# Performance work log

Hardware: AMD Instinct MI355X
Metric: run time of the kernel (lower is better)

The kernel has to match this reference:

```python
import jax, jax.numpy as jnp
import numpy as np

B, D_in, D_hid, D_out, D_future = 1024, 1024, 1024, 512, 32


def _lin_init(key, out_d, in_d, k_scale):
    k = 1.0 / np.sqrt(k_scale)
    k1, k2 = jax.random.split(key)
    W = jax.random.uniform(k1, (out_d, in_d), minval=-k, maxval=k, dtype=jnp.float32)
    b = jax.random.uniform(k2, (out_d,), minval=-k, maxval=k, dtype=jnp.float32)
    return W, b


def _lstm_cell(x, h, c, W_ih, W_hh, b_ih, b_hh):
    # PyTorch LSTMCell gate order: i, f, g, o
    gates = x @ W_ih.T + b_ih + h @ W_hh.T + b_hh
    i, f, g, o = jnp.split(gates, 4, axis=1)
    c2 = jax.nn.sigmoid(f) * c + jax.nn.sigmoid(i) * jnp.tanh(g)
    h2 = jax.nn.sigmoid(o) * jnp.tanh(c2)
    return h2, c2


def setup_inputs() -> dict:
    key = jax.random.key(0)
    ks = jax.random.split(key, 16)
    x = jax.random.normal(ks[0], (B, D_in), dtype=jnp.float32)
    hx = jax.random.normal(ks[1], (B, D_hid), dtype=jnp.float32)
    cx = jax.random.normal(ks[2], (B, D_hid), dtype=jnp.float32)
    # Decoder LSTMCell(D_out -> D_hid); torch init scale 1/sqrt(hidden)
    W_ih_dec, b_ih_dec = _lin_init(ks[3], 4 * D_hid, D_out, D_hid)
    W_hh_dec, b_hh_dec = _lin_init(ks[4], 4 * D_hid, D_hid, D_hid)
    W_r0, b_r0 = _lin_init(ks[5], D_hid, D_hid, D_hid)
    W_rp, b_rp = _lin_init(ks[6], D_out, D_hid, D_hid)
    W_rr, b_rr = _lin_init(ks[7], D_out, D_out, D_out)
    W_s0, b_s0 = _lin_init(ks[8], D_in, D_hid, D_hid)
    # StaRNNCell LSTMCell(2*D_in -> D_hid)
    W_ih_sta, b_ih_sta = _lin_init(ks[9], 4 * D_hid, 2 * D_in, D_hid)
    W_hh_sta, b_hh_sta = _lin_init(ks[10], 4 * D_hid, D_hid, D_hid)
    W_sn, b_sn = _lin_init(ks[11], D_out, D_hid, D_hid)
    return dict(x=x, hx=hx, cx=cx,
                W_ih_dec=W_ih_dec, W_hh_dec=W_hh_dec, b_ih_dec=b_ih_dec, b_hh_dec=b_hh_dec,
                W_r0=W_r0, b_r0=b_r0, W_rp=W_rp, b_rp=b_rp, W_rr=W_rr, b_rr=b_rr,
                W_s0=W_s0, b_s0=b_s0,
                W_ih_sta=W_ih_sta, W_hh_sta=W_hh_sta, b_ih_sta=b_ih_sta, b_hh_sta=b_hh_sta,
                W_sn=W_sn, b_sn=b_sn)


def reference(x, hx, cx,
              W_ih_dec, W_hh_dec, b_ih_dec, b_hh_dec,
              W_r0, b_r0, W_rp, b_rp, W_rr, b_rr,
              W_s0, b_s0,
              W_ih_sta, W_hh_sta, b_ih_sta, b_hh_sta,
              W_sn, b_sn):
    ohx, ocx = hx, cx
    r0 = jnp.zeros((x.shape[0], D_out), dtype=x.dtype)
    hd0 = hx @ W_r0.T + b_r0  # LinLayerR0

    def step(carry, _):
        r, hd, cd = carry
        hd, cd = _lstm_cell(r, hd, cd, W_ih_dec, W_hh_dec, b_ih_dec, b_hh_dec)
        p = hd @ W_rp.T + b_rp    # LinLayerRp
        r = p @ W_rr.T + b_rr     # LinLayerRr
        return (r, hd, cd), (hd, p)

    _, (fts_bar, Act_bar) = jax.lax.scan(step, (r0, hd0, cx), None, length=D_future)
    # fts_bar: [D_future, B, D_hid]; AvgPool1d over D_future == mean over axis 0
    hbar = fts_bar.mean(axis=0)
    xbar = jax.nn.relu(hbar @ W_s0.T + b_s0)  # LinLayerS0 + relu
    xcat = jnp.concatenate([x, xbar], axis=1)
    hx2, cx2 = _lstm_cell(xcat, ohx, ocx, W_ih_sta, W_hh_sta, b_ih_sta, b_hh_sta)
    Act = hx2 @ W_sn.T + b_sn  # LinLayerSn
    return (Act, Act_bar, (hx2, cx2))
```

## Files before the change

### kernel.cpp

```cpp
#include <hip/hip_runtime.h>
#include <hip/hip_bf16.h>
#include <stdint.h>


typedef unsigned short ushort_t;
typedef __attribute__((ext_vector_type(8))) short short8;
typedef __attribute__((ext_vector_type(4))) float floatx4;

__device__ __forceinline__ unsigned short f2bf(float f) {
    unsigned int u = __float_as_uint(f);
    u += 0x7FFF + ((u >> 16) & 1);
    return (unsigned short)(u >> 16);
}
__device__ __forceinline__ float bf2f(unsigned short u) {
    return __uint_as_float(((unsigned int)u) << 16);
}
__device__ __forceinline__ float sigm(float x) { return 1.f / (1.f + __expf(-x)); }

__device__ __forceinline__ void glds16(const ushort_t* g, const ushort_t* l) {
    __builtin_amdgcn_global_load_lds(
        (const __attribute__((address_space(1))) uint32_t*)g,
        (__attribute__((address_space(3))) uint32_t*)l, 16, 0, 0);
}

__device__ __forceinline__ unsigned ld_rlx(const unsigned* p) {
    return __hip_atomic_load(p, __ATOMIC_RELAXED, __HIP_MEMORY_SCOPE_AGENT);
}

template <bool WF, bool WB, bool RELU, bool NT>
__global__ __launch_bounds__(256)
void gemm_bt(const ushort_t* __restrict__ A, int lda,
             const ushort_t* __restrict__ Bw, int ldb,
             int Kloop, int kzOff,
             const float* __restrict__ bias,
             float* __restrict__ Cf, int ldcf, size_t czStride,
             ushort_t* __restrict__ Cb, int ldcb) {
    __shared__ __align__(16) ushort_t As[128 * 32];
    __shared__ __align__(16) ushort_t Bs[128 * 32];
    const int t = threadIdx.x;
    const int l = t & 63;
    const int w = t >> 6;
    int bx = blockIdx.x, by = blockIdx.y;
    if ((gridDim.y & 7) == 0) {
        const int flat = bx + gridDim.x * by;
        const int xcd = flat & 7;
        const int j = flat >> 3;
        const int jm = j / gridDim.x;
        by = xcd * (gridDim.y >> 3) + jm;
        bx = j - jm * gridDim.x;
    }
    const int m0 = by << 7;
    const int n0 = bx << 7;
    const int kz = blockIdx.z;
    A  += (size_t)kz * kzOff;
    Bw += (size_t)kz * kzOff;
    if (WF) Cf += (size_t)kz * czStride;
    const int wm = (w >> 1) << 6;
    const int wn = (w & 1) << 6;
    const int lr = l & 15;
    const int lg = l >> 4;

    floatx4 acc[4][4] = {};

    const int srow = (w << 4) + (l >> 2);
    const int cc = ((l & 3) - ((l >> 3) & 3)) & 3;
    const int scol = cc << 3;
    const ushort_t* Ag0 = A + (size_t)(m0 + srow) * lda + scol;
    const ushort_t* Ag1 = A + (size_t)(m0 + 64 + srow) * lda + scol;
    const ushort_t* Bg0 = Bw + (size_t)(n0 + srow) * ldb + scol;
    const ushort_t* Bg1 = Bw + (size_t)(n0 + 64 + srow) * ldb + scol;
    const ushort_t* lA0 = &As[t * 8];
    const ushort_t* lA1 = &As[2048 + t * 8];
    const ushort_t* lB0 = &Bs[t * 8];
    const ushort_t* lB1 = &Bs[2048 + t * 8];

    int aoff[4], boff[4];
#pragma unroll
    for (int i = 0; i < 4; i++) {
        const int Ra = wm + i * 16 + lr;
        aoff[i] = ((Ra << 2) + ((lg + ((Ra >> 1) & 3)) & 3)) << 3;
        const int Rb = wn + i * 16 + lr;
        boff[i] = ((Rb << 2) + ((lg + ((Rb >> 1) & 3)) & 3)) << 3;
    }

    for (int kk = 0; kk < Kloop; kk += 32) {
        glds16(Ag0 + kk, lA0);
        glds16(Ag1 + kk, lA1);
        glds16(Bg0 + kk, lB0);
        glds16(Bg1 + kk, lB1);
        __syncthreads();
        short8 af[4], bfr[4];
#pragma unroll
        for (int i = 0; i < 4; i++) af[i] = *(const short8*)&As[aoff[i]];
#pragma unroll
        for (int j = 0; j < 4; j++) bfr[j] = *(const short8*)&Bs[boff[j]];
#pragma unroll
        for (int i = 0; i < 4; i++)
#pragma unroll
            for (int j = 0; j < 4; j++)
                acc[i][j] = __builtin_amdgcn_mfma_f32_16x16x32_bf16(af[i], bfr[j], acc[i][j], 0, 0, 0);
        __syncthreads();
    }

#pragma unroll
    for (int i = 0; i < 4; i++) {
#pragma unroll
        for (int j = 0; j < 4; j++) {
            const int col = n0 + wn + j * 16 + lr;
            const float bv = bias ? bias[col] : 0.f;
#pragma unroll
            for (int r = 0; r < 4; r++) {
                const int row = m0 + wm + i * 16 + lg * 4 + r;
                float v = acc[i][j][r] + bv;
                if (RELU) v = fmaxf(v, 0.f);
                if (WF) {
                    if (NT) __builtin_nontemporal_store(v, &Cf[(size_t)row * ldcf + col]);
                    else Cf[(size_t)row * ldcf + col] = v;
                }
                if (WB) Cb[(size_t)row * ldcb + col] = f2bf(v);
            }
        }
    }
}

template <bool HF, bool NT>
__global__ __launch_bounds__(256, 2)
void gates_fused(const ushort_t* __restrict__ A, int lda,
                 const ushort_t* __restrict__ WI, int K,
                 const float* __restrict__ biasI,
                 const float* __restrict__ cin, float* __restrict__ cout,
                 ushort_t* __restrict__ hbf, int ldh,
                 float* __restrict__ hf) {
    __shared__ __align__(16) float Cs[64 * 132];
    ushort_t* AsBase = (ushort_t*)Cs;
    const int t = threadIdx.x;
    const int l = t & 63;
    const int w = t >> 6;
    const int flat = blockIdx.x + (blockIdx.y << 5);
    const int xcd = flat & 7;
    const int jsw = flat >> 3;
    const int bn = (xcd << 2) + (jsw >> 4);
    const int bm = jsw & 15;
    const int m0 = bm << 6;
    const int n0 = bn << 7;
    const int u0 = bn << 5;
    const int lr = l & 15;
    const int lg = l >> 4;

    floatx4 acc[4][2] = {};

    const int srow = t >> 2;
    const int cc = ((t & 3) - ((t >> 3) & 3)) & 3;
    const int scol = cc << 3;
    const ushort_t* Ag = A + (size_t)(m0 + srow) * lda + scol;

    int aoff[4];
#pragma unroll
    for (int i = 0; i < 4; i++) {
        const int Ra = i * 16 + lr;
        aoff[i] = ((Ra << 2) + ((lg + ((Ra >> 1) & 3)) & 3)) << 3;
    }
    const ushort_t* BgW[2];
#pragma unroll
    for (int jf = 0; jf < 2; jf++)
        BgW[jf] = WI + (size_t)(n0 + (w << 5) + jf * 16 + lr) * K + (lg << 3);

    auto issueA = [&](int b, int sp) {
#pragma unroll
        for (int s = 0; s < 4; s++)
            glds16(Ag + sp * 128 + s * 32, AsBase + b * 8192 + s * 2048 + t * 8);
    };
    auto loadB = [&](short8 (&br)[4][2], int sp) {
#pragma unroll
        for (int s = 0; s < 4; s++)
#pragma unroll
            for (int jf = 0; jf < 2; jf++)
                br[s][jf] = *(const short8*)(BgW[jf] + sp * 128 + s * 32);
    };
    auto compute = [&](int b, short8 (&br)[4][2]) {
#pragma unroll
        for (int s = 0; s < 4; s++) {
            short8 af[4];
#pragma unroll
            for (int i = 0; i < 4; i++)
                af[i] = *(const short8*)(AsBase + b * 8192 + s * 2048 + aoff[i]);
#pragma unroll
            for (int i = 0; i < 4; i++)
#pragma unroll
                for (int jf = 0; jf < 2; jf++)
                    acc[i][jf] = __builtin_amdgcn_mfma_f32_16x16x32_bf16(af[i], br[s][jf], acc[i][jf], 0, 0, 0);
        }
    };

    short8 b0[4][2], b1[4][2];
    const int NS = K >> 7;
    issueA(0, 0);
    loadB(b0, 0);
    for (int sp = 0; sp < NS; sp += 2) {
        __syncthreads();
        if (sp + 1 < NS) { issueA(1, sp + 1); loadB(b1, sp + 1); }
        compute(0, b0);
        __syncthreads();
        if (sp + 2 < NS) { issueA(0, sp + 2); loadB(b0, sp + 2); }
        compute(1, b1);
    }
    __syncthreads();

#pragma unroll
    for (int i = 0; i < 4; i++)
#pragma unroll
        for (int jf = 0; jf < 2; jf++) {
            const int colb = (w << 5) + jf * 16 + lr;
#pragma unroll
            for (int r = 0; r < 4; r++)
                Cs[(i * 16 + lg * 4 + r) * 132 + colb] = acc[i][jf][r];
        }
    __syncthreads();

#pragma unroll
    for (int p = 0; p < 8; p++) {
        const int row = p * 8 + (t >> 5);
        const int uu = t & 31;
        const float4 g4 = *(const float4*)&Cs[row * 132 + uu * 4];
        const int grow = m0 + row;
        const int gu = u0 + uu;
        const float4 b4 = *(const float4*)&biasI[gu * 4];
        const float iv = sigm(g4.x + b4.x);
        const float fv = sigm(g4.y + b4.y);
        const float gv = tanhf(g4.z + b4.z);
        const float ov = sigm(g4.w + b4.w);
        const size_t cidx = (size_t)grow * 1024 + gu;
        const float c = fv * cin[cidx] + iv * gv;
        const float h = ov * tanhf(c);
        if (NT) __builtin_nontemporal_store(c, &cout[cidx]);
        else cout[cidx] = c;
        hbf[(size_t)grow * ldh + gu] = f2bf(h);
        if (HF) {
            if (NT) __builtin_nontemporal_store(h, &hf[cidx]);
            else hf[cidx] = h;
        }
    }
}

__global__ __launch_bounds__(512, 1)
void gates_rows(ushort_t* __restrict__ HD,
                const ushort_t* __restrict__ Wh,
                const ushort_t* __restrict__ Wg,
                const float* __restrict__ biasD,
                const float* __restrict__ biasG,
                const float* __restrict__ cx,
                ushort_t* __restrict__ hbarb,
                unsigned* __restrict__ flags) {
    const size_t SLOT = 1048576;
    __shared__ __align__(16) float Cs[64 * 260];
    ushort_t* AsBase = (ushort_t*)Cs;
    const int t = threadIdx.x;
    const int l = t & 63;
    const int w = t >> 6;
    const int bid = blockIdx.x;
    const int g = bid >> 4;
    const int q = bid & 15;
    const int m0 = g << 6;
    const int n0 = q << 8;
    const int u0 = q << 6;
    const int lr = l & 15;
    const int lg = l >> 4;

    const int u8 = t & 255;
    const int pr = t >> 8;
    const int srow = u8 >> 2;
    const int cc = ((u8 & 3) - ((u8 >> 3) & 3)) & 3;
    const ushort_t* Ag = HD + (size_t)(m0 + srow) * 1024 + (cc << 3);

    int aoff[4];
#pragma unroll
    for (int i = 0; i < 4; i++) {
        const int Ra = i * 16 + lr;
        aoff[i] = ((Ra << 2) + ((lg + ((Ra >> 1) & 3)) & 3)) << 3;
    }

    const int uu = t & 63;
    const int gu = u0 + uu;
    const int rb = t >> 6;
    const float4 b4d = *(const float4*)&biasD[gu * 4];
    const float4 b4g = *(const float4*)&biasG[gu * 4];
    float cst[8], hsum[8];
#pragma unroll
    for (int p = 0; p < 8; p++) {
        cst[p] = cx[(size_t)(m0 + p * 8 + rb) * 1024 + gu];
        hsum[p] = 0.f;
    }

    for (int s = 0; s < 32; ++s) {
        if (s) {
            if (t < 16)
                while (ld_rlx(&flags[((g << 4) | t) << 4]) < (unsigned)s)
                    __builtin_amdgcn_s_sleep(2);
            __syncthreads();
        }

        const ushort_t* W = s ? Wg : Wh;
        const ushort_t* BgW[2];
#pragma unroll
        for (int jf = 0; jf < 2; jf++)
            BgW[jf] = W + (size_t)(n0 + (w << 5) + jf * 16 + lr) * 1024 + (lg << 3);

        floatx4 acc[4][2] = {};

        auto issueA = [&](int b, int sp) {
#pragma unroll
            for (int j = 0; j < 2; j++) {
                const int ss = pr * 2 + j;
                glds16(Ag + sp * 128 + ss * 32,
                       AsBase + b * 8192 + ss * 2048 + u8 * 8);
            }
        };
        auto loadB = [&](short8 (&br)[4][2], int sp) {
#pragma unroll
            for (int ss = 0; ss < 4; ss++)
#pragma unroll
                for (int jf = 0; jf < 2; jf++)
                    br[ss][jf] = *(const short8*)(BgW[jf] + sp * 128 + ss * 32);
        };
        auto compute = [&](int b, short8 (&br)[4][2]) {
#pragma unroll
            for (int ss = 0; ss < 4; ss++) {
                short8 af[4];
#pragma unroll
                for (int i = 0; i < 4; i++)
                    af[i] = *(const short8*)(AsBase + b * 8192 + ss * 2048 + aoff[i]);
#pragma unroll
                for (int i = 0; i < 4; i++)
#pragma unroll
                    for (int jf = 0; jf < 2; jf++)
                        acc[i][jf] = __builtin_amdgcn_mfma_f32_16x16x32_bf16(af[i], br[ss][jf], acc[i][jf], 0, 0, 0);
            }
        };

        short8 b0[4][2], b1[4][2];
        issueA(0, 0);
        loadB(b0, 0);
        for (int sp = 0; sp < 8; sp += 2) {
            __syncthreads();
            if (sp + 1 < 8) { issueA(1, sp + 1); loadB(b1, sp + 1); }
            compute(0, b0);
            __syncthreads();
            if (sp + 2 < 8) { issueA(0, sp + 2); loadB(b0, sp + 2); }
            compute(1, b1);
        }
        __syncthreads();

#pragma unroll
        for (int i = 0; i < 4; i++)
#pragma unroll
            for (int jf = 0; jf < 2; jf++) {
                const int colb = (w << 5) + jf * 16 + lr;
#pragma unroll
                for (int r = 0; r < 4; r++)
                    Cs[(i * 16 + lg * 4 + r) * 260 + colb] = acc[i][jf][r];
            }
        __syncthreads();

        ushort_t* Hout = HD + (size_t)(s + 1) * SLOT;
        const float4 b4 = s ? b4g : b4d;
#pragma unroll
        for (int p = 0; p < 8; p++) {
            const int row = p * 8 + rb;
            const float4 g4 = *(const float4*)&Cs[row * 260 + uu * 4];
            const float iv = sigm(g4.x + b4.x);
            const float fv = sigm(g4.y + b4.y);
            const float gv = tanhf(g4.z + b4.z);
            const float ov = sigm(g4.w + b4.w);
            cst[p] = fv * cst[p] + iv * gv;
            const float h = ov * tanhf(cst[p]);
            Hout[(size_t)(m0 + row) * 1024 + gu] = f2bf(h);
            hsum[p] += h;
        }

        if (s < 31) {
            __syncthreads();
            if (t == 0)
                __hip_atomic_store(&flags[((g << 4) | q) << 4], (unsigned)(s + 1),
                                   __ATOMIC_RELEASE, __HIP_MEMORY_SCOPE_AGENT);
        }
        Ag += SLOT;
    }

#pragma unroll
    for (int p = 0; p < 8; p++)
        hbarb[(size_t)(m0 + p * 8 + rb) * 1024 + gu] = f2bf(hsum[p] * (1.f / 32.f));
}

__global__ void zero_bar(unsigned* __restrict__ b, int n) {
    int i = blockIdx.x * 256 + threadIdx.x;
    if (i < n) b[i] = 0u;
}

__global__ void pack2_bf(ushort_t* __restrict__ dst, const float* __restrict__ s1, int K1,
                         const float* __restrict__ s2, int K2) {
    const int n = blockIdx.y;
    const int k = blockIdx.x * 256 + threadIdx.x;
    const int Kt = K1 + K2;
    float v = (k < K1) ? s1[(size_t)n * K1 + k] : s2[(size_t)n * K2 + (k - K1)];
    dst[(size_t)n * Kt + k] = f2bf(v);
}

__global__ void tpose_bf(ushort_t* __restrict__ dst, const float* __restrict__ src,
                         int R, int C) {
    const int c = blockIdx.y;
    const int r = blockIdx.x * 256 + threadIdx.x;
    dst[(size_t)c * R + r] = f2bf(src[(size_t)r * C + c]);
}

__global__ void ileave_whh_k(ushort_t* __restrict__ dst, const float* __restrict__ Whh) {
    const int rI = blockIdx.y;
    const int k = blockIdx.x * 256 + threadIdx.x;
    const int r = ((rI & 3) << 10) + (rI >> 2);
    dst[(size_t)rI * 1024 + k] = f2bf(Whh[(size_t)r * 1024 + k]);
}

__global__ void ileave_add_k(ushort_t* __restrict__ dst, const float* __restrict__ Wgf,
                             const float* __restrict__ Whh) {
    const int rI = blockIdx.y;
    const int k = blockIdx.x * 256 + threadIdx.x;
    const int r = ((rI & 3) << 10) + (rI >> 2);
    dst[(size_t)rI * 1024 + k] = f2bf(Wgf[(size_t)r * 1024 + k] + Whh[(size_t)r * 1024 + k]);
}

__global__ void ileave_sta_k(ushort_t* __restrict__ dst, const float* __restrict__ Wih,
                             const float* __restrict__ Whh) {
    const int rI = blockIdx.y;
    const int k = blockIdx.x * 256 + threadIdx.x;
    const int r = ((rI & 3) << 10) + (rI >> 2);
    float v = (k < 2048) ? Wih[(size_t)r * 2048 + k] : Whh[(size_t)r * 1024 + (k - 2048)];
    dst[(size_t)rI * 3072 + k] = f2bf(v);
}

__global__ void bias_il_k(float* __restrict__ dst, const float* __restrict__ b_ih,
                          const float* __restrict__ b_hh) {
    const int rI = blockIdx.x * 256 + threadIdx.x;
    const int r = ((rI & 3) << 10) + (rI >> 2);
    dst[rI] = b_ih[r] + b_hh[r];
}

__global__ void br2_k(float* __restrict__ br2, const float* __restrict__ Wrr,
                      const float* __restrict__ b_rp, const float* __restrict__ b_rr) {
    const int o = blockIdx.x * 256 + threadIdx.x;
    float s = b_rr[o];
    for (int m = 0; m < 512; m++) s += Wrr[o * 512 + m] * b_rp[m];
    br2[o] = s;
}

__global__ void biasg_k(float* __restrict__ dst, const float* __restrict__ Wih,
                        const float* __restrict__ b_ih, const float* __restrict__ b_hh,
                        const float* __restrict__ br2) {
    const int rI = blockIdx.x * 256 + threadIdx.x;
    const int r = ((rI & 3) << 10) + (rI >> 2);
    float s = b_ih[r] + b_hh[r];
    for (int o = 0; o < 512; o++) s += Wih[(size_t)r * 512 + o] * br2[o];
    dst[rI] = s;
}

__global__ void init_sta(const float* __restrict__ x, const float* __restrict__ hx,
                         ushort_t* __restrict__ A2) {
    int idx = blockIdx.x * 256 + threadIdx.x;
    int b = idx >> 10, j = idx & 1023;
    A2[(size_t)b * 3072 + j] = f2bf(x[idx]);
    A2[(size_t)b * 3072 + 2048 + j] = f2bf(hx[idx]);
}

extern "C" void kernel_launch(void* const* d_in, const int* in_sizes, int n_in,
                              void* d_out, int out_size, void* d_ws, size_t ws_size,
                              hipStream_t stream) {
    const float* x        = (const float*)d_in[0];
    const float* hx       = (const float*)d_in[1];
    const float* cx       = (const float*)d_in[2];
    const float* W_ih_dec = (const float*)d_in[3];
    const float* W_hh_dec = (const float*)d_in[4];
    const float* b_ih_dec = (const float*)d_in[5];
    const float* b_hh_dec = (const float*)d_in[6];
    const float* W_r0     = (const float*)d_in[7];
    const float* b_r0     = (const float*)d_in[8];
    const float* W_rp     = (const float*)d_in[9];
    const float* b_rp     = (const float*)d_in[10];
    const float* W_rr     = (const float*)d_in[11];
    const float* b_rr     = (const float*)d_in[12];
    const float* W_s0     = (const float*)d_in[13];
    const float* b_s0     = (const float*)d_in[14];
    const float* W_ih_sta = (const float*)d_in[15];
    const float* W_hh_sta = (const float*)d_in[16];
    const float* b_ih_sta = (const float*)d_in[17];
    const float* b_hh_sta = (const float*)d_in[18];
    const float* W_sn     = (const float*)d_in[19];
    const float* b_sn     = (const float*)d_in[20];
    float* out = (float*)d_out;

    float* Act    = out;
    float* ActBar = out + 524288;
    float* Hx2    = out + 524288 + 16777216;
    float* Cx2    = Hx2 + 1048576;

    char* ws = (char*)d_ws;
    size_t off = 0;
    auto alloc = [&](size_t bytes) -> void* {
        void* p = ws + off;
        off += (bytes + 255) & ~(size_t)255;
        return p;
    };
    const size_t SLOT = 1048576;
    ushort_t* HDall  = (ushort_t*)alloc(33ull * SLOT * 2);
    ushort_t* WgI    = (ushort_t*)alloc(4096ull * 1024 * 2);
    ushort_t* WhhI   = (ushort_t*)alloc(4096ull * 1024 * 2);
    ushort_t* WcatSI = (ushort_t*)alloc(4096ull * 3072 * 2);
    ushort_t* Wrpb   = (ushort_t*)alloc(512ull * 1024 * 2);
    ushort_t* Wr0b   = (ushort_t*)alloc(1024ull * 1024 * 2);
    ushort_t* Ws0b   = (ushort_t*)alloc(1024ull * 1024 * 2);
    ushort_t* Wsnb   = (ushort_t*)alloc(512ull * 1024 * 2);
    float*    biasDI = (float*)alloc(4096 * 4);
    float*    biasGI = (float*)alloc(4096 * 4);
    float*    biasSI = (float*)alloc(4096 * 4);
    float*    br2    = (float*)alloc(512 * 4);
    ushort_t* Acat2  = (ushort_t*)alloc(1024ull * 3072 * 2);
    ushort_t* hbarb  = (ushort_t*)alloc(1024ull * 1024 * 2);
    ushort_t* hx2b   = (ushort_t*)alloc(1024ull * 1024 * 2);
    unsigned* barws  = (unsigned*)alloc(256 * 16 * 4);
    if (ws_size < off) return;

    float*    Wgf    = (float*)(HDall + 1 * SLOT);
    ushort_t* Wihb   = HDall + 9 * SLOT;
    ushort_t* WrpT   = HDall + 11 * SLOT;
    ushort_t* Wrp2Tb = HDall + 11 * SLOT + 524288;
    ushort_t* Wrrb   = HDall + 12 * SLOT;

    zero_bar<<<16, 256, 0, stream>>>(barws, 256 * 16);
    init_sta<<<4096, 256, 0, stream>>>(x, hx, Acat2);
    pack2_bf<<<dim3(2, 512), 256, 0, stream>>>(Wrrb, W_rr, 512, nullptr, 0);
    pack2_bf<<<dim3(2, 4096), 256, 0, stream>>>(Wihb, W_ih_dec, 512, nullptr, 0);
    pack2_bf<<<dim3(4, 512), 256, 0, stream>>>(Wrpb, W_rp, 1024, nullptr, 0);
    pack2_bf<<<dim3(4, 1024), 256, 0, stream>>>(Wr0b, W_r0, 1024, nullptr, 0);
    pack2_bf<<<dim3(4, 1024), 256, 0, stream>>>(Ws0b, W_s0, 1024, nullptr, 0);
    pack2_bf<<<dim3(4, 512), 256, 0, stream>>>(Wsnb, W_sn, 1024, nullptr, 0);
    tpose_bf<<<dim3(2, 1024), 256, 0, stream>>>(WrpT, W_rp, 512, 1024);
    ileave_whh_k<<<dim3(4, 4096), 256, 0, stream>>>(WhhI, W_hh_dec);
    bias_il_k<<<16, 256, 0, stream>>>(biasDI, b_ih_dec, b_hh_dec);
    ileave_sta_k<<<dim3(12, 4096), 256, 0, stream>>>(WcatSI, W_ih_sta, W_hh_sta);
    bias_il_k<<<16, 256, 0, stream>>>(biasSI, b_ih_sta, b_hh_sta);
    br2_k<<<2, 256, 0, stream>>>(br2, W_rr, b_rp, b_rr);
    biasg_k<<<16, 256, 0, stream>>>(biasGI, W_ih_dec, b_ih_dec, b_hh_dec, br2);

    gemm_bt<false, true, false, false><<<dim3(4, 8, 1), 256, 0, stream>>>(
        WrpT, 512, Wrrb, 512, 512, 0, nullptr, nullptr, 0, 0, Wrp2Tb, 512);
    gemm_bt<true, false, false, false><<<dim3(8, 32, 1), 256, 0, stream>>>(
        Wihb, 512, Wrp2Tb, 512, 512, 0, nullptr, Wgf, 1024, 0, nullptr, 0);
    ileave_add_k<<<dim3(4, 4096), 256, 0, stream>>>(WgI, Wgf, W_hh_dec);

    gemm_bt<false, true, false, false><<<dim3(8, 8, 1), 256, 0, stream>>>(
        Acat2 + 2048, 3072, Wr0b, 1024, 1024, 0, b_r0, nullptr, 0, 0, HDall, 1024);

    gates_rows<<<256, 512, 0, stream>>>(
        HDall, WhhI, WgI, biasDI, biasGI, cx, hbarb, barws);

    gemm_bt<true, false, false, true><<<dim3(4, 256, 1), 256, 0, stream>>>(
        HDall + SLOT, 1024, Wrpb, 1024, 1024, 0, b_rp, ActBar, 512, 0, nullptr, 0);

    gemm_bt<false, true, true, false><<<dim3(8, 8, 1), 256, 0, stream>>>(
        hbarb, 1024, Ws0b, 1024, 1024, 0, b_s0, nullptr, 0, 0, Acat2 + 1024, 3072);

    gates_fused<true, true><<<dim3(32, 16), 256, 0, stream>>>(
        Acat2, 3072, WcatSI, 3072, biasSI, cx, Cx2, hx2b, 1024, Hx2);

    gemm_bt<true, false, false, true><<<dim3(4, 8, 1), 256, 0, stream>>>(
        hx2b, 1024, Wsnb, 1024, 1024, 0, b_sn, Act, 512, 0, nullptr, 0);

    (void)in_sizes; (void)n_in; (void)out_size;
}
```

Measured before the change: 1.327 ms.

## Split recurrent LSTM kernel into 32-row groups with per-span fine-grained flag polling

The persistent recurrent gates kernel now uses 512 blocks of 32 rows each instead of 256 blocks of 64 rows, halving per-block tile work and LDS use. Instead of waiting for all 16 column blocks of the row group before each step, each block polls only the two producer flags needed for the next K-span, in a rotated order starting at its own column chunk, so compute can overlap with peers still finishing. Hidden-state outputs are packed into 64-bit relaxed atomic stores and flags are published with relaxed stores after a block barrier. This relies on all 512 blocks being co-resident (launch bounds raised to 4 per CU) to avoid deadlock, and the weaker memory ordering risks visibility issues.

```diff
diff --git a/kernel.cpp b/kernel.cpp
--- a/kernel.cpp
+++ b/kernel.cpp
@@ -4,6 +4,7 @@
 
 
 typedef unsigned short ushort_t;
+typedef unsigned long long u64_t;
 typedef __attribute__((ext_vector_type(8))) short short8;
 typedef __attribute__((ext_vector_type(4))) float floatx4;
 
@@ -25,6 +26,12 @@
 
 __device__ __forceinline__ unsigned ld_rlx(const unsigned* p) {
     return __hip_atomic_load(p, __ATOMIC_RELAXED, __HIP_MEMORY_SCOPE_AGENT);
+}
+__device__ __forceinline__ void st_rlx(unsigned* p, unsigned v) {
+    __hip_atomic_store(p, v, __ATOMIC_RELAXED, __HIP_MEMORY_SCOPE_AGENT);
+}
+__device__ __forceinline__ void st_rlx64(u64_t* p, u64_t v) {
+    __hip_atomic_store(p, v, __ATOMIC_RELAXED, __HIP_MEMORY_SCOPE_AGENT);
 }
 
 template <bool WF, bool WB, bool RELU, bool NT>
@@ -242,7 +249,7 @@
     }
 }
 
-__global__ __launch_bounds__(512, 1)
+__global__ __launch_bounds__(512, 4)
 void gates_rows(ushort_t* __restrict__ HD,
                 const ushort_t* __restrict__ Wh,
                 const ushort_t* __restrict__ Wg,
@@ -252,7 +259,7 @@
                 ushort_t* __restrict__ hbarb,
                 unsigned* __restrict__ flags) {
     const size_t SLOT = 1048576;
-    __shared__ __align__(16) float Cs[64 * 260];
+    __shared__ __align__(16) float Cs[32 * 260];
     ushort_t* AsBase = (ushort_t*)Cs;
     const int t = threadIdx.x;
     const int l = t & 63;
@@ -260,77 +267,80 @@
     const int bid = blockIdx.x;
     const int g = bid >> 4;
     const int q = bid & 15;
-    const int m0 = g << 6;
+    const int m0 = g << 5;
     const int n0 = q << 8;
     const int u0 = q << 6;
     const int lr = l & 15;
     const int lg = l >> 4;
-
-    const int u8 = t & 255;
-    const int pr = t >> 8;
-    const int srow = u8 >> 2;
-    const int cc = ((u8 & 3) - ((u8 >> 3) & 3)) & 3;
+    const int fbase = g << 4;
+
+    const int u7 = t & 127;
+    const int sub = t >> 7;
+    const int srow = u7 >> 2;
+    const int cc = ((u7 & 3) - ((u7 >> 3) & 3)) & 3;
     const ushort_t* Ag = HD + (size_t)(m0 + srow) * 1024 + (cc << 3);
 
-    int aoff[4];
-#pragma unroll
-    for (int i = 0; i < 4; i++) {
+    int aoff[2];
+#pragma unroll
+    for (int i = 0; i < 2; i++) {
         const int Ra = i * 16 + lr;
         aoff[i] = ((Ra << 2) + ((lg + ((Ra >> 1) & 3)) & 3)) << 3;
     }
 
-    const int uu = t & 63;
-    const int gu = u0 + uu;
-    const int rb = t >> 6;
-    const float4 b4d = *(const float4*)&biasD[gu * 4];
-    const float4 b4g = *(const float4*)&biasG[gu * 4];
-    float cst[8], hsum[8];
-#pragma unroll
-    for (int p = 0; p < 8; p++) {
-        cst[p] = cx[(size_t)(m0 + p * 8 + rb) * 1024 + gu];
-        hsum[p] = 0.f;
-    }
-
+    const int v = t & 15;
+    const int rb = t >> 4;
+    float4 bd[4], bg[4];
+#pragma unroll
+    for (int k = 0; k < 4; k++) {
+        bd[k] = *(const float4*)&biasD[(u0 + 4 * v + k) * 4];
+        bg[k] = *(const float4*)&biasG[(u0 + 4 * v + k) * 4];
+    }
+    float cst[4], hsum[4];
+#pragma unroll
+    for (int k = 0; k < 4; k++) {
+        cst[k] = cx[(size_t)(m0 + rb) * 1024 + u0 + 4 * v + k];
+        hsum[k] = 0.f;
+    }
+
+    const int j0 = q >> 1;
     for (int s = 0; s < 32; ++s) {
-        if (s) {
-            if (t < 16)
-                while (ld_rlx(&flags[((g << 4) | t) << 4]) < (unsigned)s)
-                    __builtin_amdgcn_s_sleep(2);
-            __syncthreads();
-        }
-
         const ushort_t* W = s ? Wg : Wh;
         const ushort_t* BgW[2];
 #pragma unroll
         for (int jf = 0; jf < 2; jf++)
             BgW[jf] = W + (size_t)(n0 + (w << 5) + jf * 16 + lr) * 1024 + (lg << 3);
 
-        floatx4 acc[4][2] = {};
-
-        auto issueA = [&](int b, int sp) {
-#pragma unroll
-            for (int j = 0; j < 2; j++) {
-                const int ss = pr * 2 + j;
-                glds16(Ag + sp * 128 + ss * 32,
-                       AsBase + b * 8192 + ss * 2048 + u8 * 8);
+        floatx4 acc[2][2] = {};
+
+        auto pollSpan = [&](int sp) {
+            if (s && t < 2) {
+                const int jg = (j0 + sp) & 7;
+                while (ld_rlx(&flags[(fbase | (2 * jg + t)) << 4]) < (unsigned)s)
+                    __builtin_amdgcn_s_sleep(2);
             }
         };
+        auto issueA = [&](int b, int sp) {
+            const int jg = (j0 + sp) & 7;
+            glds16(Ag + jg * 128 + sub * 32,
+                   AsBase + b * 4096 + sub * 1024 + u7 * 8);
+        };
         auto loadB = [&](short8 (&br)[4][2], int sp) {
+            const int jg = (j0 + sp) & 7;
 #pragma unroll
             for (int ss = 0; ss < 4; ss++)
 #pragma unroll
                 for (int jf = 0; jf < 2; jf++)
-                    br[ss][jf] = *(const short8*)(BgW[jf] + sp * 128 + ss * 32);
+                    br[ss][jf] = *(const short8*)(BgW[jf] + jg * 128 + ss * 32);
         };
         auto compute = [&](int b, short8 (&br)[4][2]) {
 #pragma unroll
             for (int ss = 0; ss < 4; ss++) {
-                short8 af[4];
-#pragma unroll
-                for (int i = 0; i < 4; i++)
-                    af[i] = *(const short8*)(AsBase + b * 8192 + ss * 2048 + aoff[i]);
-#pragma unroll
-                for (int i = 0; i < 4; i++)
+                short8 af[2];
+#pragma unroll
+                for (int i = 0; i < 2; i++)
+                    af[i] = *(const short8*)(AsBase + b * 4096 + ss * 1024 + aoff[i]);
+#pragma unroll
+                for (int i = 0; i < 2; i++)
 #pragma unroll
                     for (int jf = 0; jf < 2; jf++)
                         acc[i][jf] = __builtin_amdgcn_mfma_f32_16x16x32_bf16(af[i], br[ss][jf], acc[i][jf], 0, 0, 0);
@@ -338,12 +348,16 @@
         };
 
         short8 b0[4][2], b1[4][2];
+        pollSpan(0);
+        __syncthreads();
         issueA(0, 0);
         loadB(b0, 0);
         for (int sp = 0; sp < 8; sp += 2) {
+            pollSpan(sp + 1);
             __syncthreads();
             if (sp + 1 < 8) { issueA(1, sp + 1); loadB(b1, sp + 1); }
             compute(0, b0);
+            pollSpan(sp + 2);
             __syncthreads();
             if (sp + 2 < 8) { issueA(0, sp + 2); loadB(b0, sp + 2); }
             compute(1, b1);
@@ -351,7 +365,7 @@
         __syncthreads();
 
 #pragma unroll
-        for (int i = 0; i < 4; i++)
+        for (int i = 0; i < 2; i++)
 #pragma unroll
             for (int jf = 0; jf < 2; jf++) {
                 const int colb = (w << 5) + jf * 16 + lr;
@@ -362,33 +376,35 @@
         __syncthreads();
 
         ushort_t* Hout = HD + (size_t)(s + 1) * SLOT;
-        const float4 b4 = s ? b4g : b4d;
-#pragma unroll
-        for (int p = 0; p < 8; p++) {
-            const int row = p * 8 + rb;
-            const float4 g4 = *(const float4*)&Cs[row * 260 + uu * 4];
+        u64_t pack = 0;
+#pragma unroll
+        for (int k = 0; k < 4; k++) {
+            const float4 g4 = *(const float4*)&Cs[rb * 260 + v * 16 + 4 * k];
+            const float4 b4 = s ? bg[k] : bd[k];
             const float iv = sigm(g4.x + b4.x);
             const float fv = sigm(g4.y + b4.y);
             const float gv = tanhf(g4.z + b4.z);
             const float ov = sigm(g4.w + b4.w);
-            cst[p] = fv * cst[p] + iv * gv;
-            const float h = ov * tanhf(cst[p]);
-            Hout[(size_t)(m0 + row) * 1024 + gu] = f2bf(h);
-            hsum[p] += h;
+            cst[k] = fv * cst[k] + iv * gv;
+            const float h = ov * tanhf(cst[k]);
+            pack |= ((u64_t)f2bf(h)) << (16 * k);
+            hsum[k] += h;
         }
-
-        if (s < 31) {
-            __syncthreads();
-            if (t == 0)
-                __hip_atomic_store(&flags[((g << 4) | q) << 4], (unsigned)(s + 1),
-                                   __ATOMIC_RELEASE, __HIP_MEMORY_SCOPE_AGENT);
-        }
+        u64_t* dst = (u64_t*)&Hout[(size_t)(m0 + rb) * 1024 + u0 + 4 * v];
+        if (s < 31) st_rlx64(dst, pack);
+        else *dst = pack;
+
+        __syncthreads();
+        if (s < 31 && t == 0)
+            st_rlx(&flags[(fbase | q) << 4], (unsigned)(s + 1));
         Ag += SLOT;
     }
 
-#pragma unroll
-    for (int p = 0; p < 8; p++)
-        hbarb[(size_t)(m0 + p * 8 + rb) * 1024 + gu] = f2bf(hsum[p] * (1.f / 32.f));
+    u64_t hb = 0;
+#pragma unroll
+    for (int k = 0; k < 4; k++)
+        hb |= ((u64_t)f2bf(hsum[k] * (1.f / 32.f))) << (16 * k);
+    *(u64_t*)&hbarb[(size_t)(m0 + rb) * 1024 + u0 + 4 * v] = hb;
 }
 
 __global__ void zero_bar(unsigned* __restrict__ b, int n) {
@@ -523,7 +539,7 @@
     ushort_t* Acat2  = (ushort_t*)alloc(1024ull * 3072 * 2);
     ushort_t* hbarb  = (ushort_t*)alloc(1024ull * 1024 * 2);
     ushort_t* hx2b   = (ushort_t*)alloc(1024ull * 1024 * 2);
-    unsigned* barws  = (unsigned*)alloc(256 * 16 * 4);
+    unsigned* barws  = (unsigned*)alloc(512 * 16 * 4);
     if (ws_size < off) return;
 
     float*    Wgf    = (float*)(HDall + 1 * SLOT);
@@ -532,7 +548,7 @@
     ushort_t* Wrp2Tb = HDall + 11 * SLOT + 524288;
     ushort_t* Wrrb   = HDall + 12 * SLOT;
 
-    zero_bar<<<16, 256, 0, stream>>>(barws, 256 * 16);
+    zero_bar<<<32, 256, 0, stream>>>(barws, 512 * 16);
     init_sta<<<4096, 256, 0, stream>>>(x, hx, Acat2);
     pack2_bf<<<dim3(2, 512), 256, 0, stream>>>(Wrrb, W_rr, 512, nullptr, 0);
     pack2_bf<<<dim3(2, 4096), 256, 0, stream>>>(Wihb, W_ih_dec, 512, nullptr, 0);
@@ -557,7 +573,7 @@
     gemm_bt<false, true, false, false><<<dim3(8, 8, 1), 256, 0, stream>>>(
         Acat2 + 2048, 3072, Wr0b, 1024, 1024, 0, b_r0, nullptr, 0, 0, HDall, 1024);
 
-    gates_rows<<<256, 512, 0, stream>>>(
+    gates_rows<<<512, 512, 0, stream>>>(
         HDall, WhhI, WgI, biasDI, biasGI, cx, hbarb, barws);
 
     gemm_bt<true, false, false, true><<<dim3(4, 256, 1), 256, 0, stream>>>(
```

Result: slower. 1.658 ms (+25.0%).
